# Optimization experiments

Hardware: AMD Instinct MI355X
Metric: run time of the kernel (lower is better)

Reference implementation:

```python
import jax, jax.numpy as jnp
import numpy as np

NUM_EMBEDDINGS = 512
EMBEDDING_DIM = 256
COMMITMENT_COST = 0.25


def setup_inputs() -> dict:
    key = jax.random.key(0)
    k1, k2 = jax.random.split(key)
    z_e = jax.random.normal(k1, (16, EMBEDDING_DIM, 16, 16, 16), dtype=jnp.float32)
    # codebook init: uniform(-1/K, 1/K) as in the torch module
    codebook = jax.random.uniform(
        k2, (NUM_EMBEDDINGS, EMBEDDING_DIM), dtype=jnp.float32,
        minval=-1.0 / NUM_EMBEDDINGS, maxval=1.0 / NUM_EMBEDDINGS)
    return {"z_e": z_e, "codebook": codebook}


def reference(z_e, codebook):
    # z_e: [B, C, D, H, W] -> [B, D, H, W, C]
    z_p = jnp.transpose(z_e, (0, 2, 3, 4, 1))
    spatial_shape = z_p.shape[:-1]
    flat = z_p.reshape(-1, EMBEDDING_DIM)                      # [N, C]
    z_sq = jnp.sum(flat * flat, axis=1, keepdims=True)         # [N, 1]
    cb_sq = jnp.sum(codebook * codebook, axis=1)[None, :]      # [1, K]
    dot = flat @ codebook.T                                    # [N, K]
    distances = z_sq + cb_sq - 2.0 * dot
    idx = jnp.argmin(distances, axis=1)                        # [N]
    z_q_p = codebook[idx].reshape(z_p.shape)                   # [B, D, H, W, C]
    codebook_loss = jnp.mean((z_q_p - jax.lax.stop_gradient(z_p)) ** 2)
    commitment_loss = jnp.mean((z_p - jax.lax.stop_gradient(z_q_p)) ** 2)
    vq_loss = codebook_loss + COMMITMENT_COST * commitment_loss
    # straight-through estimator
    z_q_st = z_p + jax.lax.stop_gradient(z_q_p - z_p)
    z_q = jnp.transpose(z_q_st, (0, 4, 1, 2, 3))               # [B, C, D, H, W]
    encoding_indices = idx.reshape(spatial_shape)
    return z_q, vq_loss, encoding_indices
```

## Files before the change

### kernel.cpp

```cpp
#include <hip/hip_runtime.h>

#define NPOS   65536
#define CDIM   256
#define KCODES 512
#define ZTOT   16777216
#define IDX_OFF (ZTOT + 1)
#define TAU    2.0e-3f
#define NC_FULL 0x7fff

#define WS_CBSQ 64
#define WS_CBBF 66112
#define WS_NC   132096
#define WS_DOLD 197632
#define WS_CAND 263168
#define WS_SP   787456
#define WS_RP   787712

using bf16x8 = __attribute__((ext_vector_type(8))) short;
using f32x4  = __attribute__((ext_vector_type(4))) float;

#define BARLDS() do { \
    asm volatile("s_waitcnt lgkmcnt(0)" ::: "memory"); \
    __builtin_amdgcn_s_barrier(); \
    asm volatile("" ::: "memory"); \
} while (0)

__device__ __forceinline__ unsigned short f2bf(float f) {
    unsigned int u = __float_as_uint(f);
    return (unsigned short)((u + 0x7fffu + ((u >> 16) & 1u)) >> 16);
}

__global__ void vq_cvtprep(const float* __restrict__ cb, float* __restrict__ ws) {
    const int k = blockIdx.x;
    const int c = threadIdx.x;
    __shared__ float row[256];
    __shared__ float chres[16];
    const float v = cb[(size_t)k * CDIM + c];
    row[c] = v;
    unsigned short* cbf2 = (unsigned short*)(ws + WS_CBBF);
    const int kt = c >> 5, g = (c & 31) >> 3, j = c & 7;
    cbf2[((((k >> 4) * 8 + kt) * 64) + g * 16 + (k & 15)) * 8 + j] = f2bf(v);
    __syncthreads();
    if (c < 16) {
        const float* a = &row[(c & 8) * 16];
        const int jj = c & 7;
        float r = __fmul_rn(a[jj], a[jj]);
        #pragma unroll 1
        for (int m = 1; m < 16; ++m)
            r = __fadd_rn(r, __fmul_rn(a[jj + 8 * m], a[jj + 8 * m]));
        chres[c] = r;
    }
    __syncthreads();
    if (c == 0) {
        float h0 = __fadd_rn(__fadd_rn(__fadd_rn(chres[0], chres[1]), __fadd_rn(chres[2], chres[3])),
                             __fadd_rn(__fadd_rn(chres[4], chres[5]), __fadd_rn(chres[6], chres[7])));
        float h1 = __fadd_rn(__fadd_rn(__fadd_rn(chres[8], chres[9]), __fadd_rn(chres[10], chres[11])),
                             __fadd_rn(__fadd_rn(chres[12], chres[13]), __fadd_rn(chres[14], chres[15])));
        ws[WS_CBSQ + k] = __fadd_rn(h0, h1);
    }
}

__device__ __forceinline__ void stw(unsigned short A[2][8][64][8], int nb,
                                    int c, int q, float4 v) {
    const int kt = c >> 5, gg = (c & 31) >> 3, j = c & 7;
    unsigned short* d = &A[nb][kt][gg * 16 + q * 4][j];
    d[0]  = f2bf(v.x);
    d[8]  = f2bf(v.y);
    d[16] = f2bf(v.z);
    d[24] = f2bf(v.w);
}

__launch_bounds__(512, 2)
__global__ void vq_screen(const float* __restrict__ z,
                          float* __restrict__ ws,
                          float* __restrict__ out) {
    const int t  = threadIdx.x;
    const int w  = t >> 6;
    const int l  = t & 63;
    const int g  = l >> 4;
    const int c0 = l & 15;
    int* wsi = (int*)ws;
    const unsigned short* cbf2 = (const unsigned short*)(ws + WS_CBBF);

    __shared__ unsigned short ldsA[2][8][64][8];
    __shared__ float cbsq_s[KCODES];
    __shared__ float red_v[8][16];
    __shared__ int   red_i[8][16];
    __shared__ float fv1[16];
    __shared__ int   ccnt[16];
    __shared__ int   candk[16][8];
    __shared__ float wls[8];

    cbsq_s[t] = ws[WS_CBSQ + t];
    if (t < 16) ccnt[t] = 0;

    bf16x8 bfr[4][8];
    #pragma unroll
    for (int p = 0; p < 4; ++p)
        #pragma unroll
        for (int kt = 0; kt < 8; ++kt)
            bfr[p][kt] = *(const bf16x8*)(cbf2 + ((((w * 4 + p) * 8 + kt) * 64 + l) << 3));

    const int base = blockIdx.x * 256;
    const float* zB = z + (size_t)(base >> 12) * 1048576;
    const int c1 = t >> 2, q = t & 3;

    float lsq = 0.0f;
    float lsum = 0.0f;

    {
        const float* zb = zB + (base & 4095);
        float4 a0 = *(const float4*)(zb + (size_t)c1 * 4096 + q * 4);
        float4 a1 = *(const float4*)(zb + (size_t)(c1 + 128) * 4096 + q * 4);
        stw(ldsA, 0, c1, q, a0);
        stw(ldsA, 0, c1 + 128, q, a1);
        lsq += a0.x * a0.x + a0.y * a0.y + a0.z * a0.z + a0.w * a0.w;
        lsq += a1.x * a1.x + a1.y * a1.y + a1.z * a1.z + a1.w * a1.w;
    }
    __syncthreads();

    #pragma unroll 1
    for (int it = 0; it < 16; ++it) {
        const int buf = it & 1;
        const int m0  = base + it * 16;

        float4 p0, p1;
        if (it < 15) {
            const float* zb = zB + ((m0 + 16) & 4095);
            p0 = *(const float4*)(zb + (size_t)c1 * 4096 + q * 4);
            p1 = *(const float4*)(zb + (size_t)(c1 + 128) * 4096 + q * 4);
        }

        f32x4 acc[4];
        #pragma unroll
        for (int p = 0; p < 4; ++p) acc[p] = (f32x4){0.f, 0.f, 0.f, 0.f};

        #pragma unroll
        for (int kt = 0; kt < 8; ++kt) {
            const bf16x8 a = *(const bf16x8*)&ldsA[buf][kt][l][0];
            acc[0] = __builtin_amdgcn_mfma_f32_16x16x32_bf16(a, bfr[0][kt], acc[0], 0, 0, 0);
            acc[1] = __builtin_amdgcn_mfma_f32_16x16x32_bf16(a, bfr[1][kt], acc[1], 0, 0, 0);
            acc[2] = __builtin_amdgcn_mfma_f32_16x16x32_bf16(a, bfr[2][kt], acc[2], 0, 0, 0);
            acc[3] = __builtin_amdgcn_mfma_f32_16x16x32_bf16(a, bfr[3][kt], acc[3], 0, 0, 0);
        }

        float v1[4]; int i1[4];
        #pragma unroll
        for (int r = 0; r < 4; ++r) { v1[r] = 3.4028235e38f; i1[r] = 0; }
        #pragma unroll
        for (int p = 0; p < 4; ++p) {
            const int k = w * 64 + p * 16 + c0;
            const float cq = cbsq_s[k];
            #pragma unroll
            for (int r = 0; r < 4; ++r) {
                const float s = fmaf(-2.0f, acc[p][r], cq);
                if (s < v1[r]) { v1[r] = s; i1[r] = k; }
            }
        }
        #pragma unroll
        for (int r = 0; r < 4; ++r) {
            #pragma unroll
            for (int m = 1; m < 16; m <<= 1) {
                float pv = __shfl_xor(v1[r], m, 64);
                int   pi = __shfl_xor(i1[r], m, 64);
                if (pv < v1[r] || (pv == v1[r] && pi < i1[r])) { v1[r] = pv; i1[r] = pi; }
            }
        }
        if (c0 == 0) {
            #pragma unroll
            for (int r = 0; r < 4; ++r) {
                red_v[w][g * 4 + r] = v1[r];
                red_i[w][g * 4 + r] = i1[r];
            }
        }
        BARLDS();

        if (t < 16) {
            float gv = red_v[0][t]; int gi = red_i[0][t];
            #pragma unroll
            for (int ww = 1; ww < 8; ++ww) {
                const float pv = red_v[ww][t];
                const int   pi = red_i[ww][t];
                if (pv < gv || (pv == gv && pi < gi)) { gv = pv; gi = pi; }
            }
            fv1[t] = gv;
            lsum += gv;
            out[IDX_OFF + m0 + t] = (float)gi;
        }
        BARLDS();

        #pragma unroll
        for (int p = 0; p < 4; ++p) {
            const int k = w * 64 + p * 16 + c0;
            const float cq = cbsq_s[k];
            #pragma unroll
            for (int r = 0; r < 4; ++r) {
                const float s = fmaf(-2.0f, acc[p][r], cq);
                const int row = g * 4 + r;
                if (s < fv1[row] + TAU) {
                    int pos = atomicAdd(&ccnt[row], 1);
                    if (pos < 8) candk[row][pos] = k;
                }
            }
        }
        if (it < 15) {
            stw(ldsA, buf ^ 1, c1, q, p0);
            stw(ldsA, buf ^ 1, c1 + 128, q, p1);
            lsq += p0.x * p0.x + p0.y * p0.y + p0.z * p0.z + p0.w * p0.w;
            lsq += p1.x * p1.x + p1.y * p1.y + p1.z * p1.z + p1.w * p1.w;
        }
        BARLDS();

        if (t < 16) {
            const int nc = ccnt[t];
            const int n  = m0 + t;
            wsi[WS_NC + n] = (nc > 8) ? NC_FULL : nc;
            if (nc > 1) {
                ws[WS_DOLD + n] = fv1[t];
                #pragma unroll
                for (int qq = 0; qq < 8; ++qq)
                    wsi[WS_CAND + n * 8 + qq] = (qq < nc && qq < 8) ? candk[t][qq] : 0;
            }
            ccnt[t] = 0;
        }
    }

    #pragma unroll
    for (int m = 32; m > 0; m >>= 1)
        lsq += __shfl_down(lsq, m, 64);
    if (l == 0) wls[w] = lsq;
    #pragma unroll
    for (int m = 1; m < 16; m <<= 1)
        lsum += __shfl_xor(lsum, m, 64);
    __syncthreads();
    if (t == 0) {
        float tot = ((wls[0] + wls[1]) + (wls[2] + wls[3]))
                  + ((wls[4] + wls[5]) + (wls[6] + wls[7]));
        ws[WS_SP + blockIdx.x] = tot + lsum;
    }
}

__launch_bounds__(256)
__global__ void vq_refine(const float* __restrict__ z,
                          const float* __restrict__ cb,
                          float* __restrict__ ws,
                          float* __restrict__ out) {
    const int t   = threadIdx.x;
    const int wid = t >> 6;
    const int l   = t & 63;
    int* wsi = (int*)ws;
    const int n0 = blockIdx.x * 32;

    __shared__ float zw[32][260];
    __shared__ int   snc[32];
    __shared__ float chres[32][16];
    __shared__ float zsq_s[32];
    __shared__ float wbv[4];
    __shared__ int   wbi[4];

    if (t < 32) snc[t] = wsi[WS_NC + n0 + t];

    const size_t zb = (size_t)(n0 >> 12) * 1048576 + (size_t)(n0 & 4095);
    const int rq = t & 7, ch = t >> 3;
    #pragma unroll
    for (int pass = 0; pass < 8; ++pass) {
        const int c = pass * 32 + ch;
        const float4 v = *(const float4*)(z + zb + (size_t)c * 4096 + rq * 4);
        zw[rq * 4 + 0][c] = v.x;
        zw[rq * 4 + 1][c] = v.y;
        zw[rq * 4 + 2][c] = v.z;
        zw[rq * 4 + 3][c] = v.w;
    }
    __syncthreads();

    {
        const int r = t >> 3, j = t & 7;
        #pragma unroll
        for (int h = 0; h < 2; ++h) {
            const float* a = &zw[r][h * 128];
            float rr = __fmul_rn(a[j], a[j]);
            #pragma unroll 1
            for (int m = 1; m < 16; ++m)
                rr = __fadd_rn(rr, __fmul_rn(a[j + 8 * m], a[j + 8 * m]));
            chres[r][h * 8 + j] = rr;
        }
    }
    __syncthreads();
    if (t < 32) {
        const float* cr = chres[t];
        float h0 = __fadd_rn(__fadd_rn(__fadd_rn(cr[0], cr[1]), __fadd_rn(cr[2], cr[3])),
                             __fadd_rn(__fadd_rn(cr[4], cr[5]), __fadd_rn(cr[6], cr[7])));
        float h1 = __fadd_rn(__fadd_rn(__fadd_rn(cr[8], cr[9]), __fadd_rn(cr[10], cr[11])),
                             __fadd_rn(__fadd_rn(cr[12], cr[13]), __fadd_rn(cr[14], cr[15])));
        zsq_s[t] = __fadd_rn(h0, h1);
    }
    __syncthreads();

    float bdelta = 0.0f;

    #pragma unroll 1
    for (int r = 0; r < 32; ++r) {
        const int nc = snc[r];
        if (nc <= 1) continue;
        const int n = n0 + r;
        const float zsq = zsq_s[r];
        const float4 zl = *(const float4*)&zw[r][4 * l];

        float bv = 3.4028235e38f;
        int   bi = 0x7fffffff;
        if (nc != NC_FULL) {
            for (int ci = wid; ci < nc; ci += 4) {
                const int k = wsi[WS_CAND + n * 8 + ci];
                const float4 e = *(const float4*)(cb + (size_t)k * CDIM + 4 * l);
                double d = (double)e.x * (double)zl.x + (double)e.y * (double)zl.y
                         + (double)e.z * (double)zl.z + (double)e.w * (double)zl.w;
                #pragma unroll
                for (int m = 1; m < 64; m <<= 1)
                    d += __shfl_xor(d, m, 64);
                const float dist = __fsub_rn(__fadd_rn(zsq, ws[WS_CBSQ + k]),
                                             __fmul_rn(2.0f, (float)d));
                if (dist < bv || (dist == bv && k < bi)) { bv = dist; bi = k; }
            }
        } else {
            for (int k = wid; k < KCODES; k += 4) {
                const float4 e = *(const float4*)(cb + (size_t)k * CDIM + 4 * l);
                double d = (double)e.x * (double)zl.x + (double)e.y * (double)zl.y
                         + (double)e.z * (double)zl.z + (double)e.w * (double)zl.w;
                #pragma unroll
                for (int m = 1; m < 64; m <<= 1)
                    d += __shfl_xor(d, m, 64);
                const float dist = __fsub_rn(__fadd_rn(zsq, ws[WS_CBSQ + k]),
                                             __fmul_rn(2.0f, (float)d));
                if (dist < bv || (dist == bv && k < bi)) { bv = dist; bi = k; }
            }
        }
        if (l == 0) { wbv[wid] = bv; wbi[wid] = bi; }
        __syncthreads();
        if (t == 0) {
            float v = wbv[0]; int i = wbi[0];
            #pragma unroll
            for (int ww = 1; ww < 4; ++ww) {
                if (wbv[ww] < v || (wbv[ww] == v && wbi[ww] < i)) { v = wbv[ww]; i = wbi[ww]; }
            }
            out[IDX_OFF + n] = (float)i;
            bdelta += (v - zsq) - ws[WS_DOLD + n];
        }
        __syncthreads();
    }

    if (t == 0) ws[WS_RP + blockIdx.x] = bdelta;
}

__launch_bounds__(512)
__global__ void vq_gather(const float* __restrict__ cb,
                          float* __restrict__ out) {
    __shared__ int   sidx[64];
    __shared__ float lcb[64][257];
    const int t  = threadIdx.x;
    const int n0 = blockIdx.x * 64;
    const int b  = n0 >> 12;
    const int s0 = n0 & 4095;

    if (t < 64) sidx[t] = (int)out[IDX_OFF + n0 + t];
    __syncthreads();

    {
        const int rlo = t & 7, q4 = t >> 3;
        #pragma unroll
        for (int i = 0; i < 8; ++i) {
            const int r = 8 * i + rlo;
            const float4 v = *(const float4*)(cb + (size_t)sidx[r] * CDIM + q4 * 4);
            lcb[r][q4 * 4 + 0] = v.x;
            lcb[r][q4 * 4 + 1] = v.y;
            lcb[r][q4 * 4 + 2] = v.z;
            lcb[r][q4 * 4 + 3] = v.w;
        }
    }
    __syncthreads();

    const int pq = t & 15, ch0 = t >> 4;
    const size_t obase = (size_t)b * 1048576 + (size_t)s0;
    #pragma unroll
    for (int pass = 0; pass < 8; ++pass) {
        const int c = pass * 32 + ch0;
        float4 v;
        v.x = lcb[pq * 4 + 0][c];
        v.y = lcb[pq * 4 + 1][c];
        v.z = lcb[pq * 4 + 2][c];
        v.w = lcb[pq * 4 + 3][c];
        *(float4*)(out + obase + (size_t)c * 4096 + pq * 4) = v;
    }
}

__global__ void vq_fin(const float* __restrict__ ws, float* __restrict__ out) {
    __shared__ float red[512];
    const int t = threadIdx.x;
    float s = 0.0f;
    #pragma unroll
    for (int i = t; i < 2048; i += 512) s += ws[WS_RP + i];
    if (t < 256) s += ws[WS_SP + t];
    red[t] = s;
    __syncthreads();
    for (int off = 256; off > 0; off >>= 1) {
        if (t < off) red[t] += red[t + off];
        __syncthreads();
    }
    if (t == 0)
        out[ZTOT] = 1.25f * red[0] / (float)ZTOT;
}

extern "C" void kernel_launch(void* const* d_in, const int* in_sizes, int n_in,
                              void* d_out, int out_size, void* d_ws, size_t ws_size,
                              hipStream_t stream) {
    const float* z  = (const float*)d_in[0];
    const float* cb = (const float*)d_in[1];
    float* out = (float*)d_out;
    float* ws  = (float*)d_ws;

    vq_cvtprep<<<512, 256, 0, stream>>>(cb, ws);
    vq_screen<<<NPOS / 256, 512, 0, stream>>>(z, ws, out);
    vq_refine<<<NPOS / 32, 256, 0, stream>>>(z, cb, ws, out);
    vq_gather<<<NPOS / 64, 512, 0, stream>>>(cb, out);
    vq_fin<<<1, 512, 0, stream>>>(ws, out);
}
```

Before: 137.5 us.

## Double-buffer candidate screening state to drop one barrier per tile iteration

Candidate-screening scratch (best value, counts, candidate list) becomes double-buffered, indexed by tile parity. Candidate collection for the current tile now runs after the staging barrier, and the previous tile's candidate writeback moves into the reduction step of the next iteration. This removes one block-wide barrier per iteration and overlaps the global writeback with other work. It relies on buf alternating with it, and on the final tile being flushed after the loop.

```diff
diff --git a/kernel.cpp b/kernel.cpp
--- a/kernel.cpp
+++ b/kernel.cpp
@@ -86,13 +86,13 @@
     __shared__ float cbsq_s[KCODES];
     __shared__ float red_v[8][16];
     __shared__ int   red_i[8][16];
-    __shared__ float fv1[16];
-    __shared__ int   ccnt[16];
-    __shared__ int   candk[16][8];
+    __shared__ float fv1c[2][16];
+    __shared__ int   ccnt[2][16];
+    __shared__ int   candk[2][16][8];
     __shared__ float wls[8];
 
     cbsq_s[t] = ws[WS_CBSQ + t];
-    if (t < 16) ccnt[t] = 0;
+    if (t < 32) ccnt[t >> 4][t & 15] = 0;
 
     bf16x8 bfr[4][8];
     #pragma unroll
@@ -183,24 +183,22 @@
                 const int   pi = red_i[ww][t];
                 if (pv < gv || (pv == gv && pi < gi)) { gv = pv; gi = pi; }
             }
-            fv1[t] = gv;
+            fv1c[buf][t] = gv;
             lsum += gv;
             out[IDX_OFF + m0 + t] = (float)gi;
-        }
-        BARLDS();
-
-        #pragma unroll
-        for (int p = 0; p < 4; ++p) {
-            const int k = w * 64 + p * 16 + c0;
-            const float cq = cbsq_s[k];
-            #pragma unroll
-            for (int r = 0; r < 4; ++r) {
-                const float s = fmaf(-2.0f, acc[p][r], cq);
-                const int row = g * 4 + r;
-                if (s < fv1[row] + TAU) {
-                    int pos = atomicAdd(&ccnt[row], 1);
-                    if (pos < 8) candk[row][pos] = k;
+
+            if (it > 0) {
+                const int pb = buf ^ 1;
+                const int np = m0 - 16 + t;
+                const int nc = ccnt[pb][t];
+                wsi[WS_NC + np] = (nc > 8) ? NC_FULL : nc;
+                if (nc > 1) {
+                    ws[WS_DOLD + np] = fv1c[pb][t];
+                    #pragma unroll
+                    for (int qq = 0; qq < 8; ++qq)
+                        wsi[WS_CAND + np * 8 + qq] = (qq < nc && qq < 8) ? candk[pb][t][qq] : 0;
                 }
+                ccnt[pb][t] = 0;
             }
         }
         if (it < 15) {
@@ -211,17 +209,33 @@
         }
         BARLDS();
 
-        if (t < 16) {
-            const int nc = ccnt[t];
-            const int n  = m0 + t;
-            wsi[WS_NC + n] = (nc > 8) ? NC_FULL : nc;
-            if (nc > 1) {
-                ws[WS_DOLD + n] = fv1[t];
-                #pragma unroll
-                for (int qq = 0; qq < 8; ++qq)
-                    wsi[WS_CAND + n * 8 + qq] = (qq < nc && qq < 8) ? candk[t][qq] : 0;
-            }
-            ccnt[t] = 0;
+        #pragma unroll
+        for (int p = 0; p < 4; ++p) {
+            const int k = w * 64 + p * 16 + c0;
+            const float cq = cbsq_s[k];
+            #pragma unroll
+            for (int r = 0; r < 4; ++r) {
+                const float s = fmaf(-2.0f, acc[p][r], cq);
+                const int row = g * 4 + r;
+                if (s < fv1c[buf][row] + TAU) {
+                    int pos = atomicAdd(&ccnt[buf][row], 1);
+                    if (pos < 8) candk[buf][row][pos] = k;
+                }
+            }
+        }
+    }
+
+    BARLDS();
+    if (t < 16) {
+        const int pb = 15 & 1;
+        const int np = base + 15 * 16 + t;
+        const int nc = ccnt[pb][t];
+        wsi[WS_NC + np] = (nc > 8) ? NC_FULL : nc;
+        if (nc > 1) {
+            ws[WS_DOLD + np] = fv1c[pb][t];
+            #pragma unroll
+            for (int qq = 0; qq < 8; ++qq)
+                wsi[WS_CAND + np * 8 + qq] = (qq < nc && qq < 8) ? candk[pb][t][qq] : 0;
         }
     }
 
```

New measurement: 139.6 us. No clear change (+1.5%).
